# Performance work log

Measured on AMD Instinct MI355X. Metric: run time of the kernel, lower is better.

Reference implementation:

```python
import jax, jax.numpy as jnp
import numpy as np

N, E, EMB, EDGE, ITERS = 50000, 400000, 128, 32, 2
EPS = 1e-5


def setup_inputs() -> dict:
    key = jax.random.key(0)
    ks = jax.random.split(key, 8)
    s = 0.05

    def lin(k, i, o):
        return jax.random.normal(k, (i, o), jnp.float32) * s

    def mlp_params(k):
        k1, k2 = jax.random.split(k)
        return dict(W1=lin(k1, 2 * EMB + EDGE, EMB), b1=jnp.zeros((EMB,)),
                    g1=jnp.ones((EMB,)), be1=jnp.zeros((EMB,)),
                    W2=lin(k2, EMB, EMB), b2=jnp.zeros((EMB,)),
                    g2=jnp.ones((EMB,)), be2=jnp.zeros((EMB,)))

    p = mlp_params(ks[3])
    c = mlp_params(ks[4])
    inp = {
        'nodes': jax.random.normal(ks[0], (N, EMB), jnp.float32),
        'edges': jax.random.randint(ks[1], (2, E), 0, N, jnp.int64),
        'edge_attr': jax.random.normal(ks[2], (E, EDGE), jnp.float32),
        'fW': lin(ks[5], EMB, EMB), 'fb': jnp.zeros((EMB,)),
        'fg': jnp.ones((EMB,)), 'fbe': jnp.zeros((EMB,)),
    }
    for name, d in (('p', p), ('c', c)):
        for kk, v in d.items():
            inp[name + kk] = v
    return inp


def _bn(x, g, b):
    # training-mode BatchNorm1d: batch stats over axis 0, biased variance
    m = x.mean(0)
    v = x.var(0)
    return (x - m) * jax.lax.rsqrt(v + EPS) * g + b


def _edge_mlp(h, W1, b1, g1, be1, W2, b2, g2, be2):
    h = jax.nn.relu(_bn(h @ W1 + b1, g1, be1))
    return jax.nn.relu(_bn(h @ W2 + b2, g2, be2))


def _agg(x, idx_i, idx_j, ea, params):
    # message: mlp([x_i, x_j, edge_attr]); aggregate sum at idx_i; degree-normalize
    msg = _edge_mlp(jnp.concatenate([x[idx_i], x[idx_j], ea], axis=1), *params)
    summed = jax.ops.segment_sum(msg, idx_i, num_segments=x.shape[0])
    deg = jax.ops.segment_sum(jnp.ones(idx_i.shape, x.dtype), idx_i,
                              num_segments=x.shape[0])
    deg_inv = jnp.where(deg > 0, 1.0 / deg, 0.0)
    return summed * deg_inv[:, None]


def reference(nodes, edges, edge_attr,
              pW1, pb1, pg1, pbe1, pW2, pb2, pg2, pbe2,
              cW1, cb1, cg1, cbe1, cW2, cb2, cg2, cbe2,
              fW, fb, fg, fbe):
    src, dst = edges[0], edges[1]
    pp = (pW1, pb1, pg1, pbe1, pW2, pb2, pg2, pbe2)
    cp = (cW1, cb1, cg1, cbe1, cW2, cb2, cg2, cbe2)
    for _ in range(ITERS):
        fi = _agg(nodes, dst, src, edge_attr, pp)  # parent: source_to_target
        fo = _agg(nodes, src, dst, edge_attr, cp)  # child: target_to_source
        upd = jax.nn.relu(_bn((nodes + fi + fo) @ fW + fb, fg, fbe))
        nodes = nodes + upd
    return nodes
```

## Files before the change

### kernel.cpp

```cpp
#include <hip/hip_runtime.h>
#include <math.h>

#define NN 50000
#define EE 400000
#define EMBD 128
#define KIN 288
#define NITERS 2
#define EPSV 1e-5f
#define SAE 296
#define SA1 136
#define NT_E 6250
#define G0 1024
#define G1 1024

typedef __attribute__((ext_vector_type(8))) short bf16x8;
typedef __attribute__((ext_vector_type(4))) float f32x4;

#define MFMA16(a, b, c) __builtin_amdgcn_mfma_f32_16x16x32_bf16(a, b, c, 0, 0, 0)

__device__ __forceinline__ unsigned short f2bf(float x) {
  unsigned int u = __float_as_uint(x);
  u += 0x7fffu + ((u >> 16) & 1u);
  return (unsigned short)(u >> 16);
}

__device__ __forceinline__ int physch(int ch, int row) {
  return (ch < 32) ? ((ch & ~7) | ((ch ^ (row & 7)) & 7)) : ch;
}


__global__ void k_zeroi(int* __restrict__ p, int n) {
  for (int i = blockIdx.x * blockDim.x + threadIdx.x; i < n;
       i += gridDim.x * blockDim.x)
    p[i] = 0;
}

__global__ void k_detect(const long long* __restrict__ e64, int* __restrict__ flag) {
  __shared__ int ok;
  if (threadIdx.x == 0) ok = 1;
  __syncthreads();
  for (int i = threadIdx.x; i < 4096; i += blockDim.x) {
    const long long v = e64[i];
    if (v < 0 || v >= NN) atomicAnd(&ok, 0);
  }
  __syncthreads();
  if (threadIdx.x == 0) *flag = ok;
}

__global__ void k_convert(const void* __restrict__ edges, const int* __restrict__ flag,
                          int* __restrict__ src, int* __restrict__ dst) {
  const int is64 = *flag;
  for (int i = blockIdx.x * blockDim.x + threadIdx.x; i < 2 * EE;
       i += gridDim.x * blockDim.x) {
    const int v = is64 ? (int)((const long long*)edges)[i] : ((const int*)edges)[i];
    if (i < EE) src[i] = v; else dst[i - EE] = v;
  }
}

__global__ void k_count(const int* __restrict__ src, const int* __restrict__ dst,
                        int* __restrict__ degp, int* __restrict__ degc) {
  for (int e = blockIdx.x * blockDim.x + threadIdx.x; e < EE;
       e += gridDim.x * blockDim.x) {
    atomicAdd(&degp[dst[e]], 1);
    atomicAdd(&degc[src[e]], 1);
  }
}

__global__ void k_dinv(const int* __restrict__ dp, const int* __restrict__ dc,
                       float* __restrict__ ip, float* __restrict__ ic) {
  for (int n = blockIdx.x * blockDim.x + threadIdx.x; n < NN;
       n += gridDim.x * blockDim.x) {
    ip[n] = dp[n] ? 1.f / (float)dp[n] : 0.f;
    ic[n] = dc[n] ? 1.f / (float)dc[n] : 0.f;
  }
}

__global__ __launch_bounds__(1024) void k_scan2(
    const int* __restrict__ degp, const int* __restrict__ degc,
    int* __restrict__ offp, int* __restrict__ offc) {
  const int* deg = blockIdx.x ? degc : degp;
  int* off = blockIdx.x ? offc : offp;
  __shared__ int sh[1024];
  const int t = threadIdx.x;
  const int i0 = t * 49;
  int s = 0;
#pragma unroll 1
  for (int k = 0; k < 49; ++k) {
    const int i = i0 + k;
    if (i < NN) s += deg[i];
  }
  sh[t] = s;
  __syncthreads();
  for (int o = 1; o < 1024; o <<= 1) {
    const int y = (t >= o) ? sh[t - o] : 0;
    __syncthreads();
    sh[t] += y;
    __syncthreads();
  }
  int base = sh[t] - s;
#pragma unroll 1
  for (int k = 0; k < 49; ++k) {
    const int i = i0 + k;
    if (i < NN) {
      off[i] = base;
      base += deg[i];
    }
  }
  if (t == 1023) off[NN] = sh[1023];
}

__global__ void k_copycur(const int* __restrict__ offp, const int* __restrict__ offc,
                          int* __restrict__ curp, int* __restrict__ curc) {
  for (int i = blockIdx.x * blockDim.x + threadIdx.x; i < NN;
       i += gridDim.x * blockDim.x) {
    curp[i] = offp[i];
    curc[i] = offc[i];
  }
}

__global__ void k_scatter(const int* __restrict__ src, const int* __restrict__ dst,
                          int* __restrict__ curp, int* __restrict__ curc,
                          int* __restrict__ lstp, int* __restrict__ lstc) {
  for (int e = blockIdx.x * blockDim.x + threadIdx.x; e < EE;
       e += gridDim.x * blockDim.x) {
    const int pp = atomicAdd(&curp[dst[e]], 1);
    lstp[pp] = e;
    const int pc = atomicAdd(&curc[src[e]], 1);
    lstc[pc] = e;
  }
}

__global__ void k_initnodes(const float* __restrict__ in, float* __restrict__ nd,
                            unsigned short* __restrict__ xb) {
  const int tot = NN * EMBD / 4;
  for (int i = blockIdx.x * blockDim.x + threadIdx.x; i < tot;
       i += gridDim.x * blockDim.x) {
    const float4 v = ((const float4*)in)[i];
    ((float4*)nd)[i] = v;
    short4 b;
    b.x = (short)f2bf(v.x); b.y = (short)f2bf(v.y);
    b.z = (short)f2bf(v.z); b.w = (short)f2bf(v.w);
    *(short4*)&xb[(size_t)i * 4] = b;
  }
}

__global__ void k_prepW(const float* __restrict__ W, unsigned short* __restrict__ Wt,
                        int K, int swap) {
  const int idx = blockIdx.x * blockDim.x + threadIdx.x;
  if (idx < K * EMBD) {
    const int k = idx >> 7, n = idx & 127;
    const int ksw = (swap && k < 256) ? (k ^ 128) : k;
    Wt[(size_t)n * K + ksw] = f2bf(W[(size_t)k * EMBD + n]);
  }
}

__global__ void k_prepea(const float* __restrict__ ea,
                         unsigned short* __restrict__ eab) {
  const int tot = EE * 32 / 8;
  for (int i = blockIdx.x * blockDim.x + threadIdx.x; i < tot;
       i += gridDim.x * blockDim.x) {
    const float4 a = ((const float4*)ea)[i * 2];
    const float4 b = ((const float4*)ea)[i * 2 + 1];
    union { unsigned short u[8]; uint4 v; } o;
    o.u[0] = f2bf(a.x); o.u[1] = f2bf(a.y); o.u[2] = f2bf(a.z); o.u[3] = f2bf(a.w);
    o.u[4] = f2bf(b.x); o.u[5] = f2bf(b.y); o.u[6] = f2bf(b.z); o.u[7] = f2bf(b.w);
    ((uint4*)eab)[i] = o.v;
  }
}


template <int EAB>
__global__ __launch_bounds__(256, 1) void k_pass0f(
    const unsigned short* __restrict__ xb, const int* __restrict__ idx_i,
    const int* __restrict__ idx_j, const float* __restrict__ ea,
    const unsigned short* __restrict__ eab,
    const unsigned short* __restrict__ Wp, const unsigned short* __restrict__ Wc,
    float* __restrict__ statP, float* __restrict__ statC,
    unsigned short* __restrict__ Yp, unsigned short* __restrict__ Yc) {
  __shared__ __align__(16) unsigned short Ab[64 * SAE];
  __shared__ float red[512];
  const int t = threadIdx.x;
  const int lane = t & 63, w = t >> 6, m = lane & 15, kg = lane >> 4;
  const int r = t >> 2, sub = t & 3;
  const int n0 = w * 32 + m, n1 = n0 + 16;
  bf16x8 Bp0[9], Bp1[9], Bc0[9], Bc1[9];
#pragma unroll
  for (int ks = 0; ks < 9; ++ks) {
    Bp0[ks] = *(const bf16x8*)&Wp[(size_t)n0 * KIN + ks * 32 + kg * 8];
    Bp1[ks] = *(const bf16x8*)&Wp[(size_t)n1 * KIN + ks * 32 + kg * 8];
    Bc0[ks] = *(const bf16x8*)&Wc[(size_t)n0 * KIN + ks * 32 + kg * 8];
    Bc1[ks] = *(const bf16x8*)&Wc[(size_t)n1 * KIN + ks * 32 + kg * 8];
  }
  float ps0 = 0.f, ps1 = 0.f, pq0 = 0.f, pq1 = 0.f;
  float cs0 = 0.f, cs1 = 0.f, cq0 = 0.f, cq1 = 0.f;
  int tile = blockIdx.x;
  int inext = idx_i[tile * 64 + r];
  int jnext = idx_j[tile * 64 + r];
  while (tile < NT_E) {
    const int icur = inext, jcur = jnext;
    __syncthreads();
    {
      const uint4* xi = (const uint4*)(xb + (size_t)icur * EMBD);
      const uint4* xj = (const uint4*)(xb + (size_t)jcur * EMBD);
      unsigned short* rowp = &Ab[r * SAE];
#pragma unroll
      for (int qq = 0; qq < 8; ++qq) {
        const int c = sub + qq * 4;
        const uint4 v = (c < 16) ? xi[c] : xj[c - 16];
        *(uint4*)&rowp[physch(c, r) * 8] = v;
      }
      const int e = tile * 64 + r;
      uint4 ev;
      if (EAB) {
        ev = *(const uint4*)&eab[(size_t)e * 32 + sub * 8];
      } else {
        const float4 e0 = *(const float4*)&ea[(size_t)e * 32 + sub * 8];
        const float4 e1 = *(const float4*)&ea[(size_t)e * 32 + sub * 8 + 4];
        union { unsigned short u[8]; uint4 v4; } o;
        o.u[0] = f2bf(e0.x); o.u[1] = f2bf(e0.y); o.u[2] = f2bf(e0.z);
        o.u[3] = f2bf(e0.w); o.u[4] = f2bf(e1.x); o.u[5] = f2bf(e1.y);
        o.u[6] = f2bf(e1.z); o.u[7] = f2bf(e1.w);
        ev = o.v4;
      }
      *(uint4*)&rowp[(32 + sub) * 8] = ev;
    }
    __syncthreads();
    const int next = tile + gridDim.x;
    if (next < NT_E) {
      inext = idx_i[next * 64 + r];
      jnext = idx_j[next * 64 + r];
    }
    const f32x4 zz = {0.f, 0.f, 0.f, 0.f};
    f32x4 ap[4][2] = {{zz, zz}, {zz, zz}, {zz, zz}, {zz, zz}};
    f32x4 ac[4][2] = {{zz, zz}, {zz, zz}, {zz, zz}, {zz, zz}};
#pragma unroll
    for (int ks = 0; ks < 9; ++ks) {
      const int aoff = physch(ks * 4 + kg, m) * 8;
#pragma unroll
      for (int mt = 0; mt < 4; ++mt) {
        const bf16x8 a = *(const bf16x8*)&Ab[(mt * 16 + m) * SAE + aoff];
        ap[mt][0] = MFMA16(a, Bp0[ks], ap[mt][0]);
        ap[mt][1] = MFMA16(a, Bp1[ks], ap[mt][1]);
        ac[mt][0] = MFMA16(a, Bc0[ks], ac[mt][0]);
        ac[mt][1] = MFMA16(a, Bc1[ks], ac[mt][1]);
      }
    }
#pragma unroll
    for (int mt = 0; mt < 4; ++mt)
#pragma unroll
      for (int r2 = 0; r2 < 4; ++r2) {
        const float p0 = ap[mt][0][r2], p1 = ap[mt][1][r2];
        ps0 += p0; pq0 += p0 * p0; ps1 += p1; pq1 += p1 * p1;
        const float c0 = ac[mt][0][r2], c1 = ac[mt][1][r2];
        cs0 += c0; cq0 += c0 * c0; cs1 += c1; cq1 += c1 * c1;
      }
    __syncthreads();
#pragma unroll
    for (int nt = 0; nt < 2; ++nt) {
      const int c = w * 32 + nt * 16 + m;
      const int cc = c >> 3, cl = c & 7;
#pragma unroll
      for (int mt = 0; mt < 4; ++mt)
#pragma unroll
        for (int r2 = 0; r2 < 4; ++r2) {
          const int rw = mt * 16 + kg * 4 + r2;
          Ab[rw * SAE + physch(cc, rw) * 8 + cl] = f2bf(ap[mt][nt][r2]);
          Ab[rw * SAE + physch(16 + cc, rw) * 8 + cl] = f2bf(ac[mt][nt][r2]);
        }
    }
    __syncthreads();
    unsigned short* Ytp = Yp + (size_t)tile * 64 * EMBD;
    unsigned short* Ytc = Yc + (size_t)tile * 64 * EMBD;
#pragma unroll
    for (int i = 0; i < 4; ++i) {
      const int g = i * 2048 + t * 8;
      const int row = g >> 7, ch = (g >> 3) & 15;
      *(uint4*)&Ytp[g] = *(const uint4*)&Ab[row * SAE + physch(ch, row) * 8];
      *(uint4*)&Ytc[g] = *(const uint4*)&Ab[row * SAE + physch(ch + 16, row) * 8];
    }
    tile = next;
  }
  ps0 += __shfl_xor(ps0, 16); ps0 += __shfl_xor(ps0, 32);
  pq0 += __shfl_xor(pq0, 16); pq0 += __shfl_xor(pq0, 32);
  ps1 += __shfl_xor(ps1, 16); ps1 += __shfl_xor(ps1, 32);
  pq1 += __shfl_xor(pq1, 16); pq1 += __shfl_xor(pq1, 32);
  cs0 += __shfl_xor(cs0, 16); cs0 += __shfl_xor(cs0, 32);
  cq0 += __shfl_xor(cq0, 16); cq0 += __shfl_xor(cq0, 32);
  cs1 += __shfl_xor(cs1, 16); cs1 += __shfl_xor(cs1, 32);
  cq1 += __shfl_xor(cq1, 16); cq1 += __shfl_xor(cq1, 32);
  if (kg == 0) {
    const int c0 = w * 32 + m, c1 = c0 + 16;
    red[c0] = ps0; red[128 + c0] = pq0;
    red[c1] = ps1; red[128 + c1] = pq1;
    red[256 + c0] = cs0; red[384 + c0] = cq0;
    red[256 + c1] = cs1; red[384 + c1] = cq1;
  }
  __syncthreads();
  if (t < 128) {
    atomicAdd(&statP[t], red[t]);
    atomicAdd(&statP[128 + t], red[128 + t]);
    atomicAdd(&statC[t], red[256 + t]);
    atomicAdd(&statC[128 + t], red[384 + t]);
  }
}


template <int EAB>
__global__ __launch_bounds__(256, 1) void k_pass0(
    const unsigned short* __restrict__ xb, const int* __restrict__ idx_i,
    const int* __restrict__ idx_j, const float* __restrict__ ea,
    const unsigned short* __restrict__ eab,
    const unsigned short* __restrict__ W1t, float* __restrict__ stat,
    unsigned short* __restrict__ Y1) {
  __shared__ __align__(16) unsigned short Ab[64 * SAE];
  __shared__ float red[256];
  const int t = threadIdx.x;
  const int lane = t & 63, w = t >> 6, m = lane & 15, kg = lane >> 4;
  const int r = t >> 2, sub = t & 3;
  const int n0 = w * 32 + m, n1 = n0 + 16;
  bf16x8 B0[9], B1[9];
#pragma unroll
  for (int ks = 0; ks < 9; ++ks) {
    B0[ks] = *(const bf16x8*)&W1t[(size_t)n0 * KIN + ks * 32 + kg * 8];
    B1[ks] = *(const bf16x8*)&W1t[(size_t)n1 * KIN + ks * 32 + kg * 8];
  }
  float s0 = 0.f, s1 = 0.f, q0 = 0.f, q1 = 0.f;
  int tile = blockIdx.x;
  int inext = idx_i[tile * 64 + r];
  int jnext = idx_j[tile * 64 + r];
  while (tile < NT_E) {
    const int icur = inext, jcur = jnext;
    __syncthreads();
    {
      const uint4* xi = (const uint4*)(xb + (size_t)icur * EMBD);
      const uint4* xj = (const uint4*)(xb + (size_t)jcur * EMBD);
      unsigned short* rowp = &Ab[r * SAE];
#pragma unroll
      for (int qq = 0; qq < 8; ++qq) {
        const int c = sub + qq * 4;
        const uint4 v = (c < 16) ? xi[c] : xj[c - 16];
        *(uint4*)&rowp[physch(c, r) * 8] = v;
      }
      const int e = tile * 64 + r;
      uint4 ev;
      if (EAB) {
        ev = *(const uint4*)&eab[(size_t)e * 32 + sub * 8];
      } else {
        const float4 e0 = *(const float4*)&ea[(size_t)e * 32 + sub * 8];
        const float4 e1 = *(const float4*)&ea[(size_t)e * 32 + sub * 8 + 4];
        union { unsigned short u[8]; uint4 v4; } o;
        o.u[0] = f2bf(e0.x); o.u[1] = f2bf(e0.y); o.u[2] = f2bf(e0.z);
        o.u[3] = f2bf(e0.w); o.u[4] = f2bf(e1.x); o.u[5] = f2bf(e1.y);
        o.u[6] = f2bf(e1.z); o.u[7] = f2bf(e1.w);
        ev = o.v4;
      }
      *(uint4*)&rowp[(32 + sub) * 8] = ev;
    }
    __syncthreads();
    const int next = tile + gridDim.x;
    if (next < NT_E) {
      inext = idx_i[next * 64 + r];
      jnext = idx_j[next * 64 + r];
    }
    const f32x4 zz = {0.f, 0.f, 0.f, 0.f};
    f32x4 acc[4][2] = {{zz, zz}, {zz, zz}, {zz, zz}, {zz, zz}};
#pragma unroll
    for (int ks = 0; ks < 9; ++ks) {
      const int aoff = physch(ks * 4 + kg, m) * 8;
#pragma unroll
      for (int mt = 0; mt < 4; ++mt) {
        const bf16x8 a = *(const bf16x8*)&Ab[(mt * 16 + m) * SAE + aoff];
        acc[mt][0] = MFMA16(a, B0[ks], acc[mt][0]);
        acc[mt][1] = MFMA16(a, B1[ks], acc[mt][1]);
      }
    }
#pragma unroll
    for (int mt = 0; mt < 4; ++mt)
#pragma unroll
      for (int r2 = 0; r2 < 4; ++r2) {
        const float v0 = acc[mt][0][r2], v1 = acc[mt][1][r2];
        s0 += v0; q0 += v0 * v0;
        s1 += v1; q1 += v1 * v1;
      }
    __syncthreads();
#pragma unroll
    for (int nt = 0; nt < 2; ++nt) {
      const int c = w * 32 + nt * 16 + m;
      const int cc = c >> 3, cl = c & 7;
#pragma unroll
      for (int mt = 0; mt < 4; ++mt)
#pragma unroll
        for (int r2 = 0; r2 < 4; ++r2) {
          const int rw = mt * 16 + kg * 4 + r2;
          Ab[rw * SAE + physch(cc, rw) * 8 + cl] = f2bf(acc[mt][nt][r2]);
        }
    }
    __syncthreads();
    unsigned short* Yt = Y1 + (size_t)tile * 64 * EMBD;
#pragma unroll
    for (int i = 0; i < 4; ++i) {
      const int g = i * 2048 + t * 8;
      const int row = g >> 7, ch = (g >> 3) & 15;
      *(uint4*)&Yt[g] = *(const uint4*)&Ab[row * SAE + physch(ch, row) * 8];
    }
    tile = next;
  }
  s0 += __shfl_xor(s0, 16); s0 += __shfl_xor(s0, 32);
  q0 += __shfl_xor(q0, 16); q0 += __shfl_xor(q0, 32);
  s1 += __shfl_xor(s1, 16); s1 += __shfl_xor(s1, 32);
  q1 += __shfl_xor(q1, 16); q1 += __shfl_xor(q1, 32);
  if (kg == 0) {
    const int c0 = w * 32 + m, c1 = c0 + 16;
    red[c0] = s0; red[128 + c0] = q0;
    red[c1] = s1; red[128 + c1] = q1;
  }
  __syncthreads();
  if (t < 128) {
    atomicAdd(&stat[t], red[t]);
    atomicAdd(&stat[128 + t], red[128 + t]);
  }
}


__global__ __launch_bounds__(256, 3) void k_pass1(
    const unsigned short* __restrict__ W2t, float* __restrict__ stat,
    unsigned short* __restrict__ Y) {
  __shared__ __align__(16) unsigned short Ab[64 * SA1];
  __shared__ float red[256];
  const int t = threadIdx.x;
  const int lane = t & 63, w = t >> 6, m = lane & 15, kg = lane >> 4;
  const int n0 = w * 32 + m, n1 = n0 + 16;
  const int ch = t & 15;
  bf16x8 B0[4], B1[4];
#pragma unroll
  for (int ks = 0; ks < 4; ++ks) {
    B0[ks] = *(const bf16x8*)&W2t[(size_t)n0 * EMBD + ks * 32 + kg * 8];
    B1[ks] = *(const bf16x8*)&W2t[(size_t)n1 * EMBD + ks * 32 + kg * 8];
  }
  float scr[8], shr[8];
#pragma unroll
  for (int h = 0; h < 8; ++h) {
    scr[h] = stat[256 + ch * 8 + h];
    shr[h] = stat[384 + ch * 8 + h];
  }
  float s0 = 0.f, s1 = 0.f, q0 = 0.f, q1 = 0.f;
  uint4 yreg[4];
  int tile = blockIdx.x;
  {
    const unsigned short* Yt = Y + (size_t)tile * 64 * EMBD;
#pragma unroll
    for (int i = 0; i < 4; ++i)
      yreg[i] = *(const uint4*)&Yt[i * 2048 + t * 8];
  }
  while (tile < NT_E) {
    __syncthreads();
#pragma unroll
    for (int i = 0; i < 4; ++i) {
      const int row = i * 16 + (t >> 4);
      const unsigned int* pv = (const unsigned int*)&yreg[i];
      union { unsigned short u[8]; uint4 v; } o;
#pragma unroll
      for (int h = 0; h < 4; ++h) {
        const unsigned int pw = pv[h];
        const float f0 = __uint_as_float(pw << 16);
        const float f1 = __uint_as_float(pw & 0xffff0000u);
        o.u[h * 2] = f2bf(fmaxf(fmaf(f0, scr[h * 2], shr[h * 2]), 0.f));
        o.u[h * 2 + 1] = f2bf(fmaxf(fmaf(f1, scr[h * 2 + 1], shr[h * 2 + 1]), 0.f));
      }
      *(uint4*)&Ab[row * SA1 + physch(ch, row) * 8] = o.v;
    }
    __syncthreads();
    const int next = tile + gridDim.x;
    if (next < NT_E) {
      const unsigned short* Yt = Y + (size_t)next * 64 * EMBD;
#pragma unroll
      for (int i = 0; i < 4; ++i)
        yreg[i] = *(const uint4*)&Yt[i * 2048 + t * 8];
    }
    const f32x4 zz = {0.f, 0.f, 0.f, 0.f};
    f32x4 acc[4][2] = {{zz, zz}, {zz, zz}, {zz, zz}, {zz, zz}};
#pragma unroll
    for (int ks = 0; ks < 4; ++ks) {
      const int aoff = physch(ks * 4 + kg, m) * 8;
#pragma unroll
      for (int mt = 0; mt < 4; ++mt) {
        const bf16x8 a = *(const bf16x8*)&Ab[(mt * 16 + m) * SA1 + aoff];
        acc[mt][0] = MFMA16(a, B0[ks], acc[mt][0]);
        acc[mt][1] = MFMA16(a, B1[ks], acc[mt][1]);
      }
    }
#pragma unroll
    for (int mt = 0; mt < 4; ++mt)
#pragma unroll
      for (int r2 = 0; r2 < 4; ++r2) {
        const float v0 = acc[mt][0][r2], v1 = acc[mt][1][r2];
        s0 += v0; q0 += v0 * v0;
        s1 += v1; q1 += v1 * v1;
      }
    __syncthreads();
#pragma unroll
    for (int nt = 0; nt < 2; ++nt) {
      const int c = w * 32 + nt * 16 + m;
      const int cc = c >> 3, cl = c & 7;
#pragma unroll
      for (int mt = 0; mt < 4; ++mt)
#pragma unroll
        for (int r2 = 0; r2 < 4; ++r2) {
          const int rw = mt * 16 + kg * 4 + r2;
          Ab[rw * SA1 + physch(cc, rw) * 8 + cl] = f2bf(acc[mt][nt][r2]);
        }
    }
    __syncthreads();
    unsigned short* Yo = Y + (size_t)tile * 64 * EMBD;
#pragma unroll
    for (int i = 0; i < 4; ++i) {
      const int g = i * 2048 + t * 8;
      const int row = g >> 7, c2 = (g >> 3) & 15;
      *(uint4*)&Yo[g] = *(const uint4*)&Ab[row * SA1 + physch(c2, row) * 8];
    }
    tile = next;
  }
  s0 += __shfl_xor(s0, 16); s0 += __shfl_xor(s0, 32);
  q0 += __shfl_xor(q0, 16); q0 += __shfl_xor(q0, 32);
  s1 += __shfl_xor(s1, 16); s1 += __shfl_xor(s1, 32);
  q1 += __shfl_xor(q1, 16); q1 += __shfl_xor(q1, 32);
  if (kg == 0) {
    const int c0 = w * 32 + m, c1 = c0 + 16;
    red[c0] = s0; red[128 + c0] = q0;
    red[c1] = s1; red[128 + c1] = q1;
  }
  __syncthreads();
  if (t < 128) {
    atomicAdd(&stat[512 + t], red[t]);
    atomicAdd(&stat[640 + t], red[128 + t]);
  }
}


template <int ADD>
__global__ __launch_bounds__(256) void k_agg2(
    const unsigned short* __restrict__ Y2, const int* __restrict__ off,
    const int* __restrict__ lst, const float* __restrict__ stat,
    const float* __restrict__ dinv, float* __restrict__ agg) {
  const int n = blockIdx.x * 4 + (threadIdx.x >> 6);
  const int lane = threadIdx.x & 63;
  if (n >= NN) return;
  const int o0 = off[n], o1 = off[n + 1];
  const float sc0 = stat[768 + 2 * lane], sc1 = stat[768 + 2 * lane + 1];
  const float sh0 = stat[896 + 2 * lane], sh1 = stat[896 + 2 * lane + 1];
  float a0 = 0.f, a1 = 0.f;
  for (int o = o0; o < o1; ++o) {
    const int e = lst[o];
    const unsigned int pw = ((const unsigned int*)(Y2 + (size_t)e * EMBD))[lane];
    a0 += fmaxf(fmaf(__uint_as_float(pw << 16), sc0, sh0), 0.f);
    a1 += fmaxf(fmaf(__uint_as_float(pw & 0xffff0000u), sc1, sh1), 0.f);
  }
  const float d = dinv[n];
  float2 out;
  if (ADD) {
    const float2 prev = ((const float2*)(agg + (size_t)n * EMBD))[lane];
    out.x = prev.x + a0 * d;
    out.y = prev.y + a1 * d;
  } else {
    out.x = a0 * d;
    out.y = a1 * d;
  }
  ((float2*)(agg + (size_t)n * EMBD))[lane] = out;
}


template <int NK, bool SWZ>
__device__ __forceinline__ void gemm_g(const unsigned short* Ab, const int sa,
                                       const unsigned short* __restrict__ Wt,
                                       const int K, const int m, const int kg,
                                       const int w, f32x4 acc[4][2]) {
  const int n0 = w * 32 + m, n1 = n0 + 16;
#pragma unroll
  for (int ks = 0; ks < NK; ++ks) {
    const int koff = ks * 32 + kg * 8;
    const int aoff = SWZ ? physch(koff >> 3, m) * 8 : koff;
    const bf16x8 b0 = *(const bf16x8*)&Wt[(size_t)n0 * K + koff];
    const bf16x8 b1 = *(const bf16x8*)&Wt[(size_t)n1 * K + koff];
#pragma unroll
    for (int mt = 0; mt < 4; ++mt) {
      const bf16x8 a = *(const bf16x8*)&Ab[(mt * 16 + m) * sa + aoff];
      acc[mt][0] = MFMA16(a, b0, acc[mt][0]);
      acc[mt][1] = MFMA16(a, b1, acc[mt][1]);
    }
  }
}

__device__ __forceinline__ void stats_epi64(const f32x4 acc[4][2], float* red,
                                            float* __restrict__ statg, const int t,
                                            const int m, const int kg, const int w) {
#pragma unroll
  for (int nt = 0; nt < 2; ++nt) {
    float s = 0.f, q = 0.f;
#pragma unroll
    for (int mt = 0; mt < 4; ++mt)
#pragma unroll
      for (int r = 0; r < 4; ++r) {
        const float v = acc[mt][nt][r];
        s += v;
        q += v * v;
      }
    s += __shfl_xor(s, 16); s += __shfl_xor(s, 32);
    q += __shfl_xor(q, 16); q += __shfl_xor(q, 32);
    if (kg == 0) {
      const int c = w * 32 + nt * 16 + m;
      red[c] = s;
      red[128 + c] = q;
    }
  }
  __syncthreads();
  if (t < 128) {
    atomicAdd(&statg[t], red[t]);
    atomicAdd(&statg[128 + t], red[128 + t]);
  }
}

__global__ __launch_bounds__(256) void k_node(
    const float* __restrict__ nd, float* __restrict__ ag,
    const unsigned short* __restrict__ Wt, float* __restrict__ stat) {
  __shared__ __align__(16) unsigned short Ab[64 * SA1];
  __shared__ float red[256];
  const int t = threadIdx.x;
  const int n0 = blockIdx.x * 64;
  {
    const int r = t >> 2, sub = t & 3;
    const int row = n0 + r;
    unsigned short* drow = &Ab[r * SA1];
#pragma unroll
    for (int q = 0; q < 8; ++q) {
      const int c4 = sub + q * 4;
      float4 va;
      if (row < NN) {
        va = ((const float4*)(nd + (size_t)row * EMBD))[c4];
        const float4 vb = ((const float4*)(ag + (size_t)row * EMBD))[c4];
        va.x += vb.x; va.y += vb.y; va.z += vb.z; va.w += vb.w;
      } else {
        va.x = va.y = va.z = va.w = 0.f;
      }
      short4 b;
      b.x = (short)f2bf(va.x); b.y = (short)f2bf(va.y);
      b.z = (short)f2bf(va.z); b.w = (short)f2bf(va.w);
      *(short4*)&drow[c4 * 4] = b;
    }
  }
  __syncthreads();
  const int lane = t & 63, w = t >> 6, m = lane & 15, kg = lane >> 4;
  const f32x4 zz = {0.f, 0.f, 0.f, 0.f};
  f32x4 acc[4][2] = {{zz, zz}, {zz, zz}, {zz, zz}, {zz, zz}};
  gemm_g<4, false>(Ab, SA1, Wt, EMBD, m, kg, w, acc);
#pragma unroll
  for (int nt = 0; nt < 2; ++nt) {
    const int c = w * 32 + nt * 16 + m;
#pragma unroll
    for (int mt = 0; mt < 4; ++mt)
#pragma unroll
      for (int r = 0; r < 4; ++r) {
        const int row = n0 + mt * 16 + kg * 4 + r;
        if (row < NN) ag[(size_t)row * EMBD + c] = acc[mt][nt][r];
      }
  }
  stats_epi64(acc, red, stat, t, m, kg, w);
}


__global__ void k_finalize(float* __restrict__ statbase, const float* __restrict__ g,
                           const float* __restrict__ be, float cnt) {
  const int t = threadIdx.x;
  if (t < EMBD) {
    const float s = statbase[t], sq = statbase[EMBD + t];
    const float m = s / cnt;
    float v = sq / cnt - m * m;
    v = fmaxf(v, 0.f);
    const float rs = rsqrtf(v + EPSV);
    const float sc = g[t] * rs;
    statbase[256 + t] = sc;
    statbase[384 + t] = be[t] - m * sc;
    statbase[t] = 0.f;
    statbase[EMBD + t] = 0.f;
  }
}

__global__ void k_update(float* __restrict__ nd, unsigned short* __restrict__ xb,
                         const float* __restrict__ Z, const float* __restrict__ stat) {
  const float* sc = stat + 256;
  const float* sh = stat + 384;
  const int total = NN * EMBD / 4;
  for (int i = blockIdx.x * blockDim.x + threadIdx.x; i < total;
       i += gridDim.x * blockDim.x) {
    const int c4 = i & 31;
    const float4 v = ((const float4*)Z)[i];
    const float4 s4 = ((const float4*)sc)[c4];
    const float4 h4 = ((const float4*)sh)[c4];
    float4 nv = ((float4*)nd)[i];
    nv.x += fmaxf(fmaf(v.x, s4.x, h4.x), 0.f);
    nv.y += fmaxf(fmaf(v.y, s4.y, h4.y), 0.f);
    nv.z += fmaxf(fmaf(v.z, s4.z, h4.z), 0.f);
    nv.w += fmaxf(fmaf(v.w, s4.w, h4.w), 0.f);
    ((float4*)nd)[i] = nv;
    short4 b;
    b.x = (short)f2bf(nv.x); b.y = (short)f2bf(nv.y);
    b.z = (short)f2bf(nv.z); b.w = (short)f2bf(nv.w);
    *(short4*)&xb[(size_t)i * 4] = b;
  }
}


extern "C" void kernel_launch(void* const* d_in, const int* in_sizes, int n_in,
                              void* d_out, int out_size, void* d_ws, size_t ws_size,
                              hipStream_t stream) {
  const float* in_nodes = (const float*)d_in[0];
  const void* edges = d_in[1];
  const float* ea = (const float*)d_in[2];
  const float* fW = (const float*)d_in[3];
  const float* fg = (const float*)d_in[5];
  const float* fbe = (const float*)d_in[6];
  const float* p_[8];
  const float* c_[8];
  for (int i = 0; i < 8; ++i) {
    p_[i] = (const float*)d_in[7 + i];
    c_[i] = (const float*)d_in[15 + i];
  }
  float* nodes = (float*)d_out;

  char* base = (char*)d_ws;
  size_t cur = 0;
  auto take = [&](size_t bytes) -> void* {
    void* p = base + cur;
    cur = (cur + bytes + 255) & ~(size_t)255;
    return p;
  };
  float* agg = (float*)take((size_t)NN * EMBD * 4);
  unsigned short* xb = (unsigned short*)take((size_t)NN * EMBD * 2);
  int* src = (int*)take(EE * 4);
  int* dst = (int*)take(EE * 4);
  int* lstp = (int*)take(EE * 4);
  int* lstc = (int*)take(EE * 4);
  int* offp = (int*)take((NN + 1) * 4);
  int* offc = (int*)take((NN + 1) * 4);
  int* curp = (int*)take(NN * 4);
  int* curc = (int*)take(NN * 4);
  float* dinvp = (float*)take(NN * 4);
  float* dinvc = (float*)take(NN * 4);
  float* stat = (float*)take(2048 * 4);
  int* flag = (int*)take(4);
  unsigned short* pW1t = (unsigned short*)take((size_t)EMBD * KIN * 2);
  unsigned short* pW2t = (unsigned short*)take((size_t)EMBD * EMBD * 2);
  unsigned short* cW1t = (unsigned short*)take((size_t)EMBD * KIN * 2);
  unsigned short* cW1ts = (unsigned short*)take((size_t)EMBD * KIN * 2);
  unsigned short* cW2t = (unsigned short*)take((size_t)EMBD * EMBD * 2);
  unsigned short* fWt = (unsigned short*)take((size_t)EMBD * EMBD * 2);
  unsigned short* Y1p = (unsigned short*)take((size_t)EE * EMBD * 2);
  const size_t y_bytes = (size_t)EE * EMBD * 2;
  const bool useF = (cur + y_bytes) <= ws_size;
  unsigned short* Y1c = useF ? (unsigned short*)take(y_bytes) : nullptr;
  const size_t eab_bytes = (size_t)EE * 32 * 2;
  const bool useEab = (cur + eab_bytes) <= ws_size;
  unsigned short* eab = useEab ? (unsigned short*)take(eab_bytes) : nullptr;

  k_zeroi<<<64, 256, 0, stream>>>((int*)stat, 2048);
  k_zeroi<<<128, 256, 0, stream>>>(curp, NN);
  k_zeroi<<<128, 256, 0, stream>>>(curc, NN);
  k_detect<<<1, 256, 0, stream>>>((const long long*)edges, flag);
  k_convert<<<1024, 256, 0, stream>>>(edges, flag, src, dst);
  k_count<<<1024, 256, 0, stream>>>(src, dst, curp, curc);
  k_dinv<<<128, 256, 0, stream>>>(curp, curc, dinvp, dinvc);
  k_scan2<<<2, 1024, 0, stream>>>(curp, curc, offp, offc);
  k_copycur<<<128, 256, 0, stream>>>(offp, offc, curp, curc);
  k_scatter<<<1024, 256, 0, stream>>>(src, dst, curp, curc, lstp, lstc);
  k_initnodes<<<2048, 256, 0, stream>>>(in_nodes, nodes, xb);
  k_prepW<<<(KIN * EMBD + 255) / 256, 256, 0, stream>>>(p_[0], pW1t, KIN, 0);
  k_prepW<<<(EMBD * EMBD + 255) / 256, 256, 0, stream>>>(p_[4], pW2t, EMBD, 0);
  k_prepW<<<(KIN * EMBD + 255) / 256, 256, 0, stream>>>(c_[0], cW1t, KIN, 0);
  k_prepW<<<(KIN * EMBD + 255) / 256, 256, 0, stream>>>(c_[0], cW1ts, KIN, 1);
  k_prepW<<<(EMBD * EMBD + 255) / 256, 256, 0, stream>>>(c_[4], cW2t, EMBD, 0);
  k_prepW<<<(EMBD * EMBD + 255) / 256, 256, 0, stream>>>(fW, fWt, EMBD, 0);
  if (useEab) k_prepea<<<2048, 256, 0, stream>>>(ea, eab);

  const int NB = (NN + 63) / 64;
  float* statP = stat;
  float* statC = stat + 1024;

  for (int it = 0; it < NITERS; ++it) {
    if (useF) {
      if (useEab)
        k_pass0f<1><<<G0, 256, 0, stream>>>(xb, dst, src, ea, eab, pW1t, cW1ts,
                                            statP, statC, Y1p, Y1c);
      else
        k_pass0f<0><<<G0, 256, 0, stream>>>(xb, dst, src, ea, eab, pW1t, cW1ts,
                                            statP, statC, Y1p, Y1c);
      k_finalize<<<1, 128, 0, stream>>>(statP, p_[2], p_[3], (float)EE);
      k_finalize<<<1, 128, 0, stream>>>(statC, c_[2], c_[3], (float)EE);
      k_pass1<<<G1, 256, 0, stream>>>(pW2t, statP, Y1p);
      k_finalize<<<1, 128, 0, stream>>>(statP + 512, p_[6], p_[7], (float)EE);
      k_agg2<0><<<NN / 4, 256, 0, stream>>>(Y1p, offp, lstp, statP, dinvp, agg);
      k_pass1<<<G1, 256, 0, stream>>>(cW2t, statC, Y1c);
      k_finalize<<<1, 128, 0, stream>>>(statC + 512, c_[6], c_[7], (float)EE);
      k_agg2<1><<<NN / 4, 256, 0, stream>>>(Y1c, offc, lstc, statC, dinvc, agg);
    } else {
      if (useEab)
        k_pass0<1><<<G0, 256, 0, stream>>>(xb, dst, src, ea, eab, pW1t, statP, Y1p);
      else
        k_pass0<0><<<G0, 256, 0, stream>>>(xb, dst, src, ea, eab, pW1t, statP, Y1p);
      k_finalize<<<1, 128, 0, stream>>>(statP, p_[2], p_[3], (float)EE);
      k_pass1<<<G1, 256, 0, stream>>>(pW2t, statP, Y1p);
      k_finalize<<<1, 128, 0, stream>>>(statP + 512, p_[6], p_[7], (float)EE);
      k_agg2<0><<<NN / 4, 256, 0, stream>>>(Y1p, offp, lstp, statP, dinvp, agg);
      if (useEab)
        k_pass0<1><<<G0, 256, 0, stream>>>(xb, src, dst, ea, eab, cW1t, statP, Y1p);
      else
        k_pass0<0><<<G0, 256, 0, stream>>>(xb, src, dst, ea, eab, cW1t, statP, Y1p);
      k_finalize<<<1, 128, 0, stream>>>(statP, c_[2], c_[3], (float)EE);
      k_pass1<<<G1, 256, 0, stream>>>(cW2t, statP, Y1p);
      k_finalize<<<1, 128, 0, stream>>>(statP + 512, c_[6], c_[7], (float)EE);
      k_agg2<1><<<NN / 4, 256, 0, stream>>>(Y1p, offc, lstc, statP, dinvc, agg);
    }
    k_node<<<NB, 256, 0, stream>>>(nodes, agg, fWt, statP);
    k_finalize<<<1, 128, 0, stream>>>(statP, fg, fbe, (float)NN);
    k_update<<<2048, 256, 0, stream>>>(nodes, xb, agg, statP);
  }
}
```

Before: 1.107 ms.

## Raise fused pass0 occupancy, merge parent/child pass1 and finalize launches

The fused first-layer kernel now keeps only the parent W1 fragments in registers and reloads the child W1 fragments from global/L2 on each k-step. With launch bounds raised to 3 blocks per CU and the grid grown to 1536 blocks, this trades extra weight loads for more latency hiding on the gathers. The parent and child second-layer GEMM kernels are merged into one launch of twice the grid, split by block index. Pairs of BatchNorm finalize kernels are merged into a single 256-thread launch, cutting launch overhead and letting both pass1 workloads fill the device together.

```diff
diff --git a/kernel.cpp b/kernel.cpp
--- a/kernel.cpp
+++ b/kernel.cpp
@@ -10,7 +10,7 @@
 #define SAE 296
 #define SA1 136
 #define NT_E 6250
-#define G0 1024
+#define G0 1536
 #define G1 1024
 
 typedef __attribute__((ext_vector_type(8))) short bf16x8;
@@ -170,7 +170,7 @@
 
 
 template <int EAB>
-__global__ __launch_bounds__(256, 1) void k_pass0f(
+__global__ __launch_bounds__(256, 3) void k_pass0f(
     const unsigned short* __restrict__ xb, const int* __restrict__ idx_i,
     const int* __restrict__ idx_j, const float* __restrict__ ea,
     const unsigned short* __restrict__ eab,
@@ -183,13 +183,11 @@
   const int lane = t & 63, w = t >> 6, m = lane & 15, kg = lane >> 4;
   const int r = t >> 2, sub = t & 3;
   const int n0 = w * 32 + m, n1 = n0 + 16;
-  bf16x8 Bp0[9], Bp1[9], Bc0[9], Bc1[9];
+  bf16x8 Bp0[9], Bp1[9];
 #pragma unroll
   for (int ks = 0; ks < 9; ++ks) {
     Bp0[ks] = *(const bf16x8*)&Wp[(size_t)n0 * KIN + ks * 32 + kg * 8];
     Bp1[ks] = *(const bf16x8*)&Wp[(size_t)n1 * KIN + ks * 32 + kg * 8];
-    Bc0[ks] = *(const bf16x8*)&Wc[(size_t)n0 * KIN + ks * 32 + kg * 8];
-    Bc1[ks] = *(const bf16x8*)&Wc[(size_t)n1 * KIN + ks * 32 + kg * 8];
   }
   float ps0 = 0.f, ps1 = 0.f, pq0 = 0.f, pq1 = 0.f;
   float cs0 = 0.f, cs1 = 0.f, cq0 = 0.f, cq1 = 0.f;
@@ -236,13 +234,15 @@
 #pragma unroll
     for (int ks = 0; ks < 9; ++ks) {
       const int aoff = physch(ks * 4 + kg, m) * 8;
+      const bf16x8 bc0 = *(const bf16x8*)&Wc[(size_t)n0 * KIN + ks * 32 + kg * 8];
+      const bf16x8 bc1 = *(const bf16x8*)&Wc[(size_t)n1 * KIN + ks * 32 + kg * 8];
 #pragma unroll
       for (int mt = 0; mt < 4; ++mt) {
         const bf16x8 a = *(const bf16x8*)&Ab[(mt * 16 + m) * SAE + aoff];
         ap[mt][0] = MFMA16(a, Bp0[ks], ap[mt][0]);
         ap[mt][1] = MFMA16(a, Bp1[ks], ap[mt][1]);
-        ac[mt][0] = MFMA16(a, Bc0[ks], ac[mt][0]);
-        ac[mt][1] = MFMA16(a, Bc1[ks], ac[mt][1]);
+        ac[mt][0] = MFMA16(a, bc0, ac[mt][0]);
+        ac[mt][1] = MFMA16(a, bc1, ac[mt][1]);
       }
     }
 #pragma unroll
@@ -422,9 +422,9 @@
 }
 
 
-__global__ __launch_bounds__(256, 3) void k_pass1(
+__device__ __forceinline__ void pass1_body(
     const unsigned short* __restrict__ W2t, float* __restrict__ stat,
-    unsigned short* __restrict__ Y) {
+    unsigned short* __restrict__ Y, int tile, const int stride) {
   __shared__ __align__(16) unsigned short Ab[64 * SA1];
   __shared__ float red[256];
   const int t = threadIdx.x;
@@ -445,7 +445,6 @@
   }
   float s0 = 0.f, s1 = 0.f, q0 = 0.f, q1 = 0.f;
   uint4 yreg[4];
-  int tile = blockIdx.x;
   {
     const unsigned short* Yt = Y + (size_t)tile * 64 * EMBD;
 #pragma unroll
@@ -470,7 +469,7 @@
       *(uint4*)&Ab[row * SA1 + physch(ch, row) * 8] = o.v;
     }
     __syncthreads();
-    const int next = tile + gridDim.x;
+    const int next = tile + stride;
     if (next < NT_E) {
       const unsigned short* Yt = Y + (size_t)next * 64 * EMBD;
 #pragma unroll
@@ -534,6 +533,23 @@
     atomicAdd(&stat[512 + t], red[t]);
     atomicAdd(&stat[640 + t], red[128 + t]);
   }
+}
+
+__global__ __launch_bounds__(256, 3) void k_pass1(
+    const unsigned short* __restrict__ W2t, float* __restrict__ stat,
+    unsigned short* __restrict__ Y) {
+  pass1_body(W2t, stat, Y, blockIdx.x, G1);
+}
+
+__global__ __launch_bounds__(256, 3) void k_pass1m(
+    const unsigned short* __restrict__ Wp, const unsigned short* __restrict__ Wc,
+    float* __restrict__ statP, float* __restrict__ statC,
+    unsigned short* __restrict__ Yp, unsigned short* __restrict__ Yc) {
+  const int phase = (blockIdx.x >= G1) ? 1 : 0;
+  const unsigned short* W2t = phase ? Wc : Wp;
+  float* stat = phase ? statC : statP;
+  unsigned short* Y = phase ? Yc : Yp;
+  pass1_body(W2t, stat, Y, blockIdx.x - phase * G1, G1);
 }
 
 
@@ -667,21 +683,35 @@
 }
 
 
+__device__ __forceinline__ void finalize_one(float* __restrict__ sb,
+                                             const float* __restrict__ g,
+                                             const float* __restrict__ be,
+                                             float cnt, int c) {
+  const float s = sb[c], sq = sb[EMBD + c];
+  const float m = s / cnt;
+  float v = sq / cnt - m * m;
+  v = fmaxf(v, 0.f);
+  const float rs = rsqrtf(v + EPSV);
+  const float sc = g[c] * rs;
+  sb[256 + c] = sc;
+  sb[384 + c] = be[c] - m * sc;
+  sb[c] = 0.f;
+  sb[EMBD + c] = 0.f;
+}
+
 __global__ void k_finalize(float* __restrict__ statbase, const float* __restrict__ g,
                            const float* __restrict__ be, float cnt) {
   const int t = threadIdx.x;
-  if (t < EMBD) {
-    const float s = statbase[t], sq = statbase[EMBD + t];
-    const float m = s / cnt;
-    float v = sq / cnt - m * m;
-    v = fmaxf(v, 0.f);
-    const float rs = rsqrtf(v + EPSV);
-    const float sc = g[t] * rs;
-    statbase[256 + t] = sc;
-    statbase[384 + t] = be[t] - m * sc;
-    statbase[t] = 0.f;
-    statbase[EMBD + t] = 0.f;
-  }
+  if (t < EMBD) finalize_one(statbase, g, be, cnt, t);
+}
+
+__global__ void k_finalize2(float* __restrict__ sA, const float* __restrict__ gA,
+                            const float* __restrict__ bA, float* __restrict__ sB,
+                            const float* __restrict__ gB, const float* __restrict__ bB,
+                            float cnt) {
+  const int t = threadIdx.x;
+  if (t < EMBD) finalize_one(sA, gA, bA, cnt, t);
+  else finalize_one(sB, gB, bB, cnt, t - EMBD);
 }
 
 __global__ void k_update(float* __restrict__ nd, unsigned short* __restrict__ xb,
@@ -792,27 +822,26 @@
       else
         k_pass0f<0><<<G0, 256, 0, stream>>>(xb, dst, src, ea, eab, pW1t, cW1ts,
                                             statP, statC, Y1p, Y1c);
-      k_finalize<<<1, 128, 0, stream>>>(statP, p_[2], p_[3], (float)EE);
-      k_finalize<<<1, 128, 0, stream>>>(statC, c_[2], c_[3], (float)EE);
-      k_pass1<<<G1, 256, 0, stream>>>(pW2t, statP, Y1p);
-      k_finalize<<<1, 128, 0, stream>>>(statP + 512, p_[6], p_[7], (float)EE);
+      k_finalize2<<<1, 256, 0, stream>>>(statP, p_[2], p_[3],
+                                         statC, c_[2], c_[3], (float)EE);
+      k_pass1m<<<2 * G1, 256, 0, stream>>>(pW2t, cW2t, statP, statC, Y1p, Y1c);
+      k_finalize2<<<1, 256, 0, stream>>>(statP + 512, p_[6], p_[7],
+                                         statC + 512, c_[6], c_[7], (float)EE);
       k_agg2<0><<<NN / 4, 256, 0, stream>>>(Y1p, offp, lstp, statP, dinvp, agg);
-      k_pass1<<<G1, 256, 0, stream>>>(cW2t, statC, Y1c);
-      k_finalize<<<1, 128, 0, stream>>>(statC + 512, c_[6], c_[7], (float)EE);
       k_agg2<1><<<NN / 4, 256, 0, stream>>>(Y1c, offc, lstc, statC, dinvc, agg);
     } else {
       if (useEab)
-        k_pass0<1><<<G0, 256, 0, stream>>>(xb, dst, src, ea, eab, pW1t, statP, Y1p);
+        k_pass0<1><<<G1, 256, 0, stream>>>(xb, dst, src, ea, eab, pW1t, statP, Y1p);
       else
-        k_pass0<0><<<G0, 256, 0, stream>>>(xb, dst, src, ea, eab, pW1t, statP, Y1p);
+        k_pass0<0><<<G1, 256, 0, stream>>>(xb, dst, src, ea, eab, pW1t, statP, Y1p);
       k_finalize<<<1, 128, 0, stream>>>(statP, p_[2], p_[3], (float)EE);
       k_pass1<<<G1, 256, 0, stream>>>(pW2t, statP, Y1p);
       k_finalize<<<1, 128, 0, stream>>>(statP + 512, p_[6], p_[7], (float)EE);
       k_agg2<0><<<NN / 4, 256, 0, stream>>>(Y1p, offp, lstp, statP, dinvp, agg);
       if (useEab)
-        k_pass0<1><<<G0, 256, 0, stream>>>(xb, src, dst, ea, eab, cW1t, statP, Y1p);
+        k_pass0<1><<<G1, 256, 0, stream>>>(xb, src, dst, ea, eab, cW1t, statP, Y1p);
       else
-        k_pass0<0><<<G0, 256, 0, stream>>>(xb, src, dst, ea, eab, cW1t, statP, Y1p);
+        k_pass0<0><<<G1, 256, 0, stream>>>(xb, src, dst, ea, eab, cW1t, statP, Y1p);
       k_finalize<<<1, 128, 0, stream>>>(statP, c_[2], c_[3], (float)EE);
       k_pass1<<<G1, 256, 0, stream>>>(cW2t, statP, Y1p);
       k_finalize<<<1, 128, 0, stream>>>(statP + 512, c_[6], c_[7], (float)EE);
```

After: 1.612 ms. 1.46x slower.
